# Optimization experiments

Measured on AMD Instinct MI355X. Metric: run time of the kernel, lower is better.

Reference implementation:

```python
import math
import jax, jax.numpy as jnp
import numpy as np

N, DIN, DOUT = 32768, 1024, 1024
C = 1.0            # ball curvature c (k = -c)
MIN_NORM = 1e-15
EPS_PROJ = 4e-3    # geoopt float32 boundary eps


def _safe_norm(x):
    # sqrt of clipped sum-of-squares: finite value and finite grad at 0
    return jnp.sqrt(jnp.clip(jnp.sum(x * x, axis=-1, keepdims=True), MIN_NORM))


def _artanh(u):
    return jnp.arctanh(jnp.clip(u, -1.0 + 1e-5, 1.0 - 1e-5))


def _project(x, c):
    norm = _safe_norm(x)
    maxnorm = (1.0 - EPS_PROJ) / jnp.sqrt(c)
    return jnp.where(norm > maxnorm, x / norm * maxnorm, x)


def _mobius_matvec(W, x, c):
    sqc = jnp.sqrt(c)
    x_norm = _safe_norm(x)                       # [N,1]
    mx = x @ W.T                                 # [N,DOUT]
    mx_norm = _safe_norm(mx)                     # [N,1]
    res = jnp.tanh(mx_norm / x_norm * _artanh(sqc * x_norm)) * mx / (mx_norm * sqc)
    zero = jnp.all(mx == 0, axis=-1, keepdims=True)
    return jnp.where(zero, jnp.zeros((), x.dtype), res)


def _expmap0(u, c):
    sqc = jnp.sqrt(c)
    u_norm = _safe_norm(u)
    return jnp.tanh(sqc * u_norm) * u / (sqc * u_norm)


def _mobius_add(x, y, c):
    x2 = jnp.sum(x * x, axis=-1, keepdims=True)
    y2 = jnp.sum(y * y, axis=-1, keepdims=True)
    xy = jnp.sum(x * y, axis=-1, keepdims=True)
    num = (1.0 + 2.0 * c * xy + c * y2) * x + (1.0 - c * x2) * y
    denom = 1.0 + 2.0 * c * xy + c * c * x2 * y2
    return num / jnp.clip(denom, MIN_NORM)


def setup_inputs() -> dict:
    key = jax.random.key(0)
    kx, kw, kb = jax.random.split(key, 3)
    x = jax.random.normal(kx, (N, DIN), jnp.float32)
    # place points strictly inside the unit Poincare ball
    x = x / (jnp.linalg.norm(x, axis=-1, keepdims=True) + 1.0) * 0.7
    limit = math.sqrt(2.0) * math.sqrt(6.0 / (DIN + DOUT))  # xavier_uniform gain=sqrt(2)
    weight = jax.random.uniform(kw, (DOUT, DIN), jnp.float32, -limit, limit)
    bias = 0.01 * jax.random.normal(kb, (DOUT,), jnp.float32)
    return {"x": x, "weight": weight, "bias": bias}


def reference(x, weight, bias) -> jnp.ndarray:
    c = jnp.float32(C)
    res = _mobius_matvec(weight, x, c)           # dropout=0 / eval: weight used as-is
    res = _project(res, c)
    hyp_bias = _project(_expmap0(bias[None, :], c), c)
    res = _project(_mobius_add(res, hyp_bias, c), c)
    return res
```

## Files before the change

### kernel.cpp

```cpp
#include <hip/hip_runtime.h>
#include <hip/hip_bf16.h>
#include <cmath>

#define NROWS 32768
#define DIN   1024
#define DOUT  1024
#define BM    64
#define BK    32
#define NKT   (DIN / BK)
#define MAXNORM 0.996f
#define XPAD  40

typedef __attribute__((ext_vector_type(8))) __bf16 bf16x8;
typedef __attribute__((ext_vector_type(4))) float  f32x4;
typedef __attribute__((ext_vector_type(2))) float  f32x2;
typedef __attribute__((ext_vector_type(4))) unsigned u32x4;

__device__ __forceinline__ unsigned pack2bf(float a, float b) {
    union { unsigned u; __bf16 h[2]; } p;
    p.h[0] = (__bf16)a; p.h[1] = (__bf16)b;
    return p.u;
}

__global__ void conv_w_kernel(const float* __restrict__ Wf, __bf16* __restrict__ Wb) {
    int c  = blockIdx.x * blockDim.x + threadIdx.x;
    int l  = c & 63;
    int j  = (c >> 6) & 63;
    int kt = c >> 12;
    int n  = j * 16 + (l & 15);
    int k0 = kt * 32 + (l >> 4) * 8;
    const float* src = Wf + (size_t)n * DIN + k0;
    f32x4 v0 = *(const f32x4*)src;
    f32x4 v1 = *(const f32x4*)(src + 4);
    u32x4 o;
    o.x = pack2bf(v0[0], v0[1]); o.y = pack2bf(v0[2], v0[3]);
    o.z = pack2bf(v1[0], v1[1]); o.w = pack2bf(v1[2], v1[3]);
    *(u32x4*)((char*)Wb + (size_t)c * 16) = o;
}

__global__ __launch_bounds__(1024) void hyp_kernel_reg(
    const float* __restrict__ X,
    const __bf16* __restrict__ Wb,
    const float* __restrict__ bias,
    float* __restrict__ out)
{
    __shared__ __align__(16) __bf16 Xt[4][BM * XPAD];
    __shared__ float hbs[DOUT];
    __shared__ float xsqs[BM];
    __shared__ float fco[BM][2];
    __shared__ float bred[16];

    const int tid  = threadIdx.x;
    const int lane = tid & 63;
    const int wid  = tid >> 6;
    const int l15  = lane & 15;
    const int l4   = lane >> 4;
    const int row0 = blockIdx.x * BM;
    const int kt0  = (blockIdx.x >> 3) & 31;

    const int xr = tid >> 4;
    const int xk = (tid & 15) * 2;
    const float* xp = X + (size_t)(row0 + xr) * DIN + xk;
    float xsq = 0.f;

    const __bf16* wp = Wb + ((size_t)(wid * 4) * 64 + lane) * 8;

    auto ktOf = [&](int s) { return (kt0 + s) & 31; };

    f32x4 acc[4][4];
    #pragma unroll
    for (int m = 0; m < 4; m++)
        #pragma unroll
        for (int n = 0; n < 4; n++)
            acc[m][n] = (f32x4){0.f, 0.f, 0.f, 0.f};

    f32x2 x0 = *(const f32x2*)(xp + (size_t)ktOf(0) * BK);
    f32x2 x1 = *(const f32x2*)(xp + (size_t)ktOf(1) * BK);
    bf16x8 bfr[4];
    {
        const __bf16* wkp = wp + (size_t)ktOf(0) * 32768;
        #pragma unroll
        for (int i = 0; i < 4; i++) bfr[i] = *(const bf16x8*)(wkp + i * 512);
    }

    float bv = bias[tid];
    float bs = bv * bv;
    #pragma unroll
    for (int m = 1; m < 64; m <<= 1) bs += __shfl_xor(bs, m);
    if (lane == 0) bred[wid] = bs;
    __syncthreads();
    float tot = 0.f;
    #pragma unroll
    for (int i = 0; i < 16; i++) tot += bred[i];
    const float bnorm = sqrtf(fmaxf(tot, 1e-15f));
    const float bth   = tanhf(bnorm);
    float sc0 = bth / bnorm;
    float hn  = bth;
    if (hn > MAXNORM) { sc0 *= MAXNORM / hn; hn = MAXNORM; }
    hbs[tid] = sc0 * bv;
    const float y2c = hn * hn;

    xsq += x0[0] * x0[0] + x0[1] * x0[1];
    *(unsigned*)((char*)(&Xt[0][0]) + xr * (XPAD * 2) + xk * 2) = pack2bf(x0[0], x0[1]);
    x0 = x1;
    x1 = *(const f32x2*)(xp + (size_t)ktOf(2) * BK);

    auto step = [&](int s, int rb, int wb) {
        if (s + 1 < NKT) {
            xsq += x0[0] * x0[0] + x0[1] * x0[1];
            *(unsigned*)((char*)(&Xt[wb][0]) + xr * (XPAD * 2) + xk * 2) = pack2bf(x0[0], x0[1]);
        }
        x0 = x1;
        int sf = s + 3 < NKT ? s + 3 : NKT - 1;
        x1 = *(const f32x2*)(xp + (size_t)ktOf(sf) * BK);

        asm volatile("s_waitcnt lgkmcnt(0)" ::: "memory");
        __builtin_amdgcn_s_barrier();
        __builtin_amdgcn_sched_barrier(0);

        const char* xb = (const char*)(&Xt[rb][0]);
        bf16x8 a[4];
        #pragma unroll
        for (int m = 0; m < 4; m++)
            a[m] = *(const bf16x8*)(xb + ((m << 4) + l15) * (XPAD * 2) + (l4 << 4));

        __builtin_amdgcn_s_setprio(1);
        #pragma unroll
        for (int n = 0; n < 4; n++)
            #pragma unroll
            for (int m = 0; m < 4; m++)
                acc[m][n] = __builtin_amdgcn_mfma_f32_16x16x32_bf16(a[m], bfr[n], acc[m][n], 0, 0, 0);
        __builtin_amdgcn_s_setprio(0);

        int sb = s + 1 < NKT ? s + 1 : NKT - 1;
        const __bf16* wkp = wp + (size_t)ktOf(sb) * 32768;
        #pragma unroll
        for (int i = 0; i < 4; i++) bfr[i] = *(const bf16x8*)(wkp + i * 512);
    };

    for (int s = 0; s < NKT; s += 4) {
        step(s + 0, 0, 1);
        step(s + 1, 1, 2);
        step(s + 2, 2, 3);
        step(s + 3, 3, 0);
    }

    __syncthreads();

    float* redq = (float*)(&Xt[0][0]);
    float* redd = redq + BM * 16;

    float xs = xsq;
    #pragma unroll
    for (int m = 1; m < 16; m <<= 1) xs += __shfl_xor(xs, m);
    if (l15 == 0) xsqs[xr] = xs;

    float hv[4];
    #pragma unroll
    for (int n = 0; n < 4; n++) hv[n] = hbs[(wid << 6) + (n << 4) + l15];

    #pragma unroll
    for (int m = 0; m < 4; m++) {
        #pragma unroll
        for (int r = 0; r < 4; r++) {
            float s = 0.f, d = 0.f;
            #pragma unroll
            for (int n = 0; n < 4; n++) {
                float v = acc[m][n][r];
                s += v * v;
                d += v * hv[n];
            }
            #pragma unroll
            for (int mm = 1; mm < 16; mm <<= 1) {
                s += __shfl_xor(s, mm);
                d += __shfl_xor(d, mm);
            }
            if (l15 == 0) {
                int rl = (m << 4) + (l4 << 2) + r;
                redq[rl * 16 + wid] = s;
                redd[rl * 16 + wid] = d;
            }
        }
    }
    __syncthreads();

    if (tid < BM) {
        int r = tid;
        float sq = 0.f, dt = 0.f;
        #pragma unroll
        for (int w = 0; w < 16; w++) { sq += redq[r * 16 + w]; dt += redd[r * 16 + w]; }
        float sx     = xsqs[r];
        float xnorm  = sqrtf(fmaxf(sx, 1e-15f));
        float mxnorm = sqrtf(fmaxf(sq, 1e-15f));
        float u  = fminf(xnorm, 1.f - 1e-5f);
        float tv = tanhf(mxnorm / xnorm * atanhf(u));
        float rn = fminf(tv, MAXNORM);
        float s  = rn / mxnorm;
        float xy = s * dt;
        float x2 = rn * rn;
        float Am = 1.f + 2.f * xy + y2c;
        float Bm = 1.f - x2;
        float Dm = fmaxf(1.f + 2.f * xy + x2 * y2c, 1e-15f);
        float g1 = Am * s / Dm;
        float g2 = Bm / Dm;
        float osq   = g1 * g1 * sq + 2.f * g1 * g2 * dt + g2 * g2 * y2c;
        float onorm = sqrtf(fmaxf(osq, 1e-15f));
        float psc   = onorm > MAXNORM ? MAXNORM / onorm : 1.f;
        fco[r][0] = g1 * psc;
        fco[r][1] = g2 * psc;
    }
    __syncthreads();

    #pragma unroll
    for (int m = 0; m < 4; m++) {
        #pragma unroll
        for (int r = 0; r < 4; r++) {
            int rl = (m << 4) + (l4 << 2) + r;
            float F1 = fco[rl][0], F2 = fco[rl][1];
            float* orow = out + (size_t)(row0 + rl) * DOUT + (wid << 6);
            #pragma unroll
            for (int n = 0; n < 4; n++)
                orow[(n << 4) + l15] = F1 * acc[m][n][r] + F2 * hv[n];
        }
    }
}

__global__ __launch_bounds__(512, 2) void hyp_kernel_basic(
    const float* __restrict__ X,
    const float* __restrict__ Wf,
    const float* __restrict__ bias,
    float* __restrict__ out)
{
    __shared__ __align__(16) __bf16 Wt[2][DOUT * BK];
    __shared__ __align__(16) __bf16 Xt[2][BM * XPAD];
    __shared__ float hbs[DOUT];
    __shared__ float redq[BM][8];
    __shared__ float redd[BM][8];
    __shared__ float xsqs[BM];
    __shared__ float fco[BM][2];
    __shared__ float bred[8];

    const int tid  = threadIdx.x;
    const int lane = tid & 63;
    const int wid  = tid >> 6;
    const int l15  = lane & 15;
    const int l4   = lane >> 4;
    const int row0 = blockIdx.x * BM;
    const int xr = tid >> 3;
    const int xk = (tid & 7) * 4;
    const float* xp = X + (size_t)(row0 + xr) * DIN + xk;
    float xsq = 0.f;

    f32x4 acc[4][8];
    #pragma unroll
    for (int m = 0; m < 4; m++)
        #pragma unroll
        for (int nt = 0; nt < 8; nt++)
            acc[m][nt] = (f32x4){0.f, 0.f, 0.f, 0.f};

    auto STAGE = [&](int buf, int kt) {
        if (kt < NKT) {
            #pragma unroll
            for (int j = 0; j < 8; j++) {
                int c = (j << 9) + tid;
                int q = c & 3, n = c >> 2;
                int k0 = kt * BK + ((q ^ ((n >> 1) & 3)) << 3);
                const float* src = Wf + (size_t)n * DIN + k0;
                f32x4 v0 = *(const f32x4*)src;
                f32x4 v1 = *(const f32x4*)(src + 4);
                u32x4 o;
                o.x = pack2bf(v0[0], v0[1]); o.y = pack2bf(v0[2], v0[3]);
                o.z = pack2bf(v1[0], v1[1]); o.w = pack2bf(v1[2], v1[3]);
                *(u32x4*)((char*)(&Wt[buf][0]) + c * 16) = o;
            }
            f32x4 xv = *(const f32x4*)(xp + kt * BK);
            xsq += xv[0]*xv[0] + xv[1]*xv[1] + xv[2]*xv[2] + xv[3]*xv[3];
            uint2 pk;
            pk.x = pack2bf(xv[0], xv[1]);
            pk.y = pack2bf(xv[2], xv[3]);
            *(uint2*)((char*)(&Xt[buf][0]) + xr * (XPAD * 2) + xk * 2) = pk;
        }
    };

    STAGE(0, 0);

    float b0 = bias[tid], b1 = bias[tid + 512];
    float bs = b0 * b0 + b1 * b1;
    #pragma unroll
    for (int m = 1; m < 64; m <<= 1) bs += __shfl_xor(bs, m);
    if (lane == 0) bred[wid] = bs;
    __syncthreads();
    float tot = 0.f;
    #pragma unroll
    for (int i = 0; i < 8; i++) tot += bred[i];
    const float bnorm = sqrtf(fmaxf(tot, 1e-15f));
    const float bth   = tanhf(bnorm);
    float sc0 = bth / bnorm;
    float hn  = bth;
    if (hn > MAXNORM) { sc0 *= MAXNORM / hn; hn = MAXNORM; }
    hbs[tid]       = sc0 * b0;
    hbs[tid + 512] = sc0 * b1;
    const float y2c = hn * hn;
    __syncthreads();

    float hv[8];
    #pragma unroll
    for (int nt = 0; nt < 8; nt++) hv[nt] = hbs[(wid << 7) + (nt << 4) + l15];

    int cur = 0;
    for (int kt = 0; kt < NKT; kt++) {
        STAGE(cur ^ 1, kt + 1);
        const char* xb = (const char*)(&Xt[cur][0]);
        const char* wb = (const char*)(&Wt[cur][0]);
        bf16x8 a[4], b[8];
        #pragma unroll
        for (int m = 0; m < 4; m++)
            a[m] = *(const bf16x8*)(xb + ((m << 4) + l15) * (XPAD * 2) + (l4 << 4));
        #pragma unroll
        for (int nt = 0; nt < 8; nt++) {
            int n = (wid << 7) + (nt << 4) + l15;
            b[nt] = *(const bf16x8*)(wb + n * 64 + ((l4 ^ ((n >> 1) & 3)) << 4));
        }
        #pragma unroll
        for (int m = 0; m < 4; m++)
            #pragma unroll
            for (int nt = 0; nt < 8; nt++)
                acc[m][nt] = __builtin_amdgcn_mfma_f32_16x16x32_bf16(a[m], b[nt], acc[m][nt], 0, 0, 0);
        __syncthreads();
        cur ^= 1;
    }

    float xs = xsq;
    #pragma unroll
    for (int m = 1; m < 8; m <<= 1) xs += __shfl_xor(xs, m);
    if ((tid & 7) == 0) xsqs[xr] = xs;

    #pragma unroll
    for (int m = 0; m < 4; m++) {
        #pragma unroll
        for (int r = 0; r < 4; r++) {
            float s = 0.f, d = 0.f;
            #pragma unroll
            for (int nt = 0; nt < 8; nt++) {
                float v = acc[m][nt][r];
                s += v * v;
                d += v * hv[nt];
            }
            #pragma unroll
            for (int mm = 1; mm < 16; mm <<= 1) {
                s += __shfl_xor(s, mm);
                d += __shfl_xor(d, mm);
            }
            if (l15 == 0) {
                int rl = (m << 4) + (l4 << 2) + r;
                redq[rl][wid] = s;
                redd[rl][wid] = d;
            }
        }
    }
    __syncthreads();

    if (tid < BM) {
        int r = tid;
        float sq = 0.f, dt = 0.f;
        #pragma unroll
        for (int w = 0; w < 8; w++) { sq += redq[r][w]; dt += redd[r][w]; }
        float sx     = xsqs[r];
        float xnorm  = sqrtf(fmaxf(sx, 1e-15f));
        float mxnorm = sqrtf(fmaxf(sq, 1e-15f));
        float u  = fminf(xnorm, 1.f - 1e-5f);
        float tv = tanhf(mxnorm / xnorm * atanhf(u));
        float rn = fminf(tv, MAXNORM);
        float s  = rn / mxnorm;
        float xy = s * dt;
        float x2 = rn * rn;
        float Am = 1.f + 2.f * xy + y2c;
        float Bm = 1.f - x2;
        float Dm = fmaxf(1.f + 2.f * xy + x2 * y2c, 1e-15f);
        float g1 = Am * s / Dm;
        float g2 = Bm / Dm;
        float osq   = g1 * g1 * sq + 2.f * g1 * g2 * dt + g2 * g2 * y2c;
        float onorm = sqrtf(fmaxf(osq, 1e-15f));
        float psc   = onorm > MAXNORM ? MAXNORM / onorm : 1.f;
        fco[r][0] = g1 * psc;
        fco[r][1] = g2 * psc;
    }
    __syncthreads();

    #pragma unroll
    for (int m = 0; m < 4; m++) {
        #pragma unroll
        for (int r = 0; r < 4; r++) {
            int rl = (m << 4) + (l4 << 2) + r;
            float F1 = fco[rl][0], F2 = fco[rl][1];
            float* orow = out + (size_t)(row0 + rl) * DOUT + (wid << 7);
            #pragma unroll
            for (int nt = 0; nt < 8; nt++)
                orow[(nt << 4) + l15] = F1 * acc[m][nt][r] + F2 * hv[nt];
        }
    }
}

extern "C" void kernel_launch(void* const* d_in, const int* in_sizes, int n_in,
                              void* d_out, int out_size, void* d_ws, size_t ws_size,
                              hipStream_t stream) {
    const float* X    = (const float*)d_in[0];
    const float* W    = (const float*)d_in[1];
    const float* bias = (const float*)d_in[2];
    float* out = (float*)d_out;

    const size_t wb_bytes = (size_t)DOUT * DIN * 2;
    if (ws_size >= wb_bytes) {
        __bf16* Wb = (__bf16*)d_ws;
        conv_w_kernel<<<dim3(512), dim3(256), 0, stream>>>(W, Wb);
        hyp_kernel_reg<<<dim3(NROWS / BM), dim3(1024), 0, stream>>>(X, Wb, bias, out);
    } else {
        hyp_kernel_basic<<<dim3(NROWS / BM), dim3(512), 0, stream>>>(X, W, bias, out);
    }
}
```

Before: 121.0 us.

## Stage weight tiles via global_load_lds double buffer instead of register loads

Replaces the per-wave direct global-to-register loads of the bf16 weight fragments with asynchronous global_load_lds DMA into a double-buffered LDS staging area, then reads the B fragments from LDS before the MFMAs. It also drops the per-block rotation of the starting k-tile, so every block walks K in the same order. The aim is to hide global load latency behind compute and cut VGPR pressure. In exchange it adds 128 KB of LDS, which may limit occupancy to one block per CU. The vmcnt(6) wait count has to line up with the buffers still in flight, and with only a single barrier per step the staging buffers risk write-after-read hazards.

```diff
diff --git a/kernel.cpp b/kernel.cpp
--- a/kernel.cpp
+++ b/kernel.cpp
@@ -15,6 +15,12 @@
 typedef __attribute__((ext_vector_type(4))) float  f32x4;
 typedef __attribute__((ext_vector_type(2))) float  f32x2;
 typedef __attribute__((ext_vector_type(4))) unsigned u32x4;
+
+__device__ __forceinline__ void gload16(const void* g, void* l) {
+    __builtin_amdgcn_global_load_lds(
+        (const __attribute__((address_space(1))) void*)g,
+        (__attribute__((address_space(3))) void*)l, 16, 0, 0);
+}
 
 __device__ __forceinline__ unsigned pack2bf(float a, float b) {
     union { unsigned u; __bf16 h[2]; } p;
@@ -38,12 +44,13 @@
     *(u32x4*)((char*)Wb + (size_t)c * 16) = o;
 }
 
-__global__ __launch_bounds__(1024) void hyp_kernel_reg(
+__global__ __launch_bounds__(1024) void hyp_kernel_ldsb(
     const float* __restrict__ X,
     const __bf16* __restrict__ Wb,
     const float* __restrict__ bias,
     float* __restrict__ out)
 {
+    __shared__ __align__(16) __bf16 Bst[2][DOUT * BK];
     __shared__ __align__(16) __bf16 Xt[4][BM * XPAD];
     __shared__ float hbs[DOUT];
     __shared__ float xsqs[BM];
@@ -56,16 +63,22 @@
     const int l15  = lane & 15;
     const int l4   = lane >> 4;
     const int row0 = blockIdx.x * BM;
-    const int kt0  = (blockIdx.x >> 3) & 31;
 
     const int xr = tid >> 4;
     const int xk = (tid & 15) * 2;
     const float* xp = X + (size_t)(row0 + xr) * DIN + xk;
     float xsq = 0.f;
 
-    const __bf16* wp = Wb + ((size_t)(wid * 4) * 64 + lane) * 8;
-
-    auto ktOf = [&](int s) { return (kt0 + s) & 31; };
+    const char* wsrc = (const char*)Wb + ((size_t)((wid << 2) * 64 + lane)) * 16;
+    char* bdst0 = (char*)(&Bst[0][0]) + (wid << 12);
+    char* bdst1 = (char*)(&Bst[1][0]) + (wid << 12);
+
+    auto dmaB = [&](int kt, char* dst) {
+        const char* s = wsrc + ((size_t)kt << 16);
+        #pragma unroll
+        for (int i = 0; i < 4; i++)
+            gload16(s + (i << 10), dst + (i << 10));
+    };
 
     f32x4 acc[4][4];
     #pragma unroll
@@ -74,14 +87,10 @@
         for (int n = 0; n < 4; n++)
             acc[m][n] = (f32x4){0.f, 0.f, 0.f, 0.f};
 
-    f32x2 x0 = *(const f32x2*)(xp + (size_t)ktOf(0) * BK);
-    f32x2 x1 = *(const f32x2*)(xp + (size_t)ktOf(1) * BK);
-    bf16x8 bfr[4];
-    {
-        const __bf16* wkp = wp + (size_t)ktOf(0) * 32768;
-        #pragma unroll
-        for (int i = 0; i < 4; i++) bfr[i] = *(const bf16x8*)(wkp + i * 512);
-    }
+    dmaB(0, bdst0);
+    __builtin_amdgcn_sched_barrier(0);
+    f32x2 x0 = *(const f32x2*)xp;
+    f32x2 x1 = *(const f32x2*)(xp + BK);
 
     float bv = bias[tid];
     float bs = bv * bv;
@@ -103,16 +112,20 @@
     xsq += x0[0] * x0[0] + x0[1] * x0[1];
     *(unsigned*)((char*)(&Xt[0][0]) + xr * (XPAD * 2) + xk * 2) = pack2bf(x0[0], x0[1]);
     x0 = x1;
-    x1 = *(const f32x2*)(xp + (size_t)ktOf(2) * BK);
-
-    auto step = [&](int s, int rb, int wb) {
+    x1 = *(const f32x2*)(xp + 2 * BK);
+
+    auto step = [&](int s, int rb, int wb, int pb) {
+        int sb = s + 1 < NKT ? s + 1 : NKT - 1;
+        dmaB(sb, pb ? bdst0 : bdst1);
+        __builtin_amdgcn_sched_barrier(0);
+
         if (s + 1 < NKT) {
             xsq += x0[0] * x0[0] + x0[1] * x0[1];
             *(unsigned*)((char*)(&Xt[wb][0]) + xr * (XPAD * 2) + xk * 2) = pack2bf(x0[0], x0[1]);
         }
         x0 = x1;
         int sf = s + 3 < NKT ? s + 3 : NKT - 1;
-        x1 = *(const f32x2*)(xp + (size_t)ktOf(sf) * BK);
+        x1 = *(const f32x2*)(xp + (size_t)sf * BK);
 
         asm volatile("s_waitcnt lgkmcnt(0)" ::: "memory");
         __builtin_amdgcn_s_barrier();
@@ -124,25 +137,28 @@
         for (int m = 0; m < 4; m++)
             a[m] = *(const bf16x8*)(xb + ((m << 4) + l15) * (XPAD * 2) + (l4 << 4));
 
+        asm volatile("s_waitcnt vmcnt(6)" ::: "memory");
+        __builtin_amdgcn_sched_barrier(0);
+        const char* bb = (const char*)(pb ? bdst1 : bdst0);
+        bf16x8 b[4];
+        #pragma unroll
+        for (int i = 0; i < 4; i++)
+            b[i] = *(const bf16x8*)(bb + (i << 10) + (lane << 4));
+
         __builtin_amdgcn_s_setprio(1);
         #pragma unroll
         for (int n = 0; n < 4; n++)
             #pragma unroll
             for (int m = 0; m < 4; m++)
-                acc[m][n] = __builtin_amdgcn_mfma_f32_16x16x32_bf16(a[m], bfr[n], acc[m][n], 0, 0, 0);
+                acc[m][n] = __builtin_amdgcn_mfma_f32_16x16x32_bf16(a[m], b[n], acc[m][n], 0, 0, 0);
         __builtin_amdgcn_s_setprio(0);
-
-        int sb = s + 1 < NKT ? s + 1 : NKT - 1;
-        const __bf16* wkp = wp + (size_t)ktOf(sb) * 32768;
-        #pragma unroll
-        for (int i = 0; i < 4; i++) bfr[i] = *(const bf16x8*)(wkp + i * 512);
     };
 
     for (int s = 0; s < NKT; s += 4) {
-        step(s + 0, 0, 1);
-        step(s + 1, 1, 2);
-        step(s + 2, 2, 3);
-        step(s + 3, 3, 0);
+        step(s + 0, 0, 1, 0);
+        step(s + 1, 1, 2, 1);
+        step(s + 2, 2, 3, 0);
+        step(s + 3, 3, 0, 1);
     }
 
     __syncthreads();
@@ -413,7 +429,7 @@
     if (ws_size >= wb_bytes) {
         __bf16* Wb = (__bf16*)d_ws;
         conv_w_kernel<<<dim3(512), dim3(256), 0, stream>>>(W, Wb);
-        hyp_kernel_reg<<<dim3(NROWS / BM), dim3(1024), 0, stream>>>(X, Wb, bias, out);
+        hyp_kernel_ldsb<<<dim3(NROWS / BM), dim3(1024), 0, stream>>>(X, Wb, bias, out);
     } else {
         hyp_kernel_basic<<<dim3(NROWS / BM), dim3(512), 0, stream>>>(X, W, bias, out);
     }
```

Result: slower. 163.1 us (+34.8%).
